# Performance work log

Hardware: AMD Instinct MI355X
Metric: run time of the kernel (lower is better)

The kernel has to match this reference:

```python
import jax, jax.numpy as jnp
import numpy as np

EPS = 1e-6
THRESHOLD = 0.99
MAX_STEPS = 4
MIN_STEPS = 1
N_HEAD = 8
B, N, D, V, L, F, RCF = 1, 256, 512, 32000, 2, 1536, 2048


def rmsnorm(x, w):
    return x * jax.lax.rsqrt(jnp.mean(x * x, axis=-1, keepdims=True) + EPS) * w


def rope(x, base=10000.0):
    # x: [B, N, H, hd] -> rotary embedding (rotate-half convention)
    n, hd = x.shape[1], x.shape[-1]
    half = hd // 2
    inv = 1.0 / (base ** (jnp.arange(half, dtype=jnp.float32) * 2.0 / hd))
    ang = jnp.arange(n, dtype=jnp.float32)[:, None] * inv[None, :]  # [N, half]
    cos = jnp.cos(ang)[None, :, None, :]
    sin = jnp.sin(ang)[None, :, None, :]
    x1, x2 = x[..., :half], x[..., half:]
    return jnp.concatenate([x1 * cos - x2 * sin, x1 * sin + x2 * cos], axis=-1)


def attention(x, wqkv, wo):
    b, n, d = x.shape
    hd = d // N_HEAD
    q, k, v = jnp.split(x @ wqkv, 3, axis=-1)
    q = rope(q.reshape(b, n, N_HEAD, hd))
    k = rope(k.reshape(b, n, N_HEAD, hd))
    v = v.reshape(b, n, N_HEAD, hd)
    scores = jnp.einsum('bqhd,bkhd->bhqk', q, k) / np.float32(np.sqrt(hd))
    causal = jnp.tril(jnp.ones((n, n), dtype=bool))
    scores = jnp.where(causal, scores, jnp.float32(-1e30))
    a = jax.nn.softmax(scores, axis=-1)
    out = jnp.einsum('bhqk,bkhd->bqhd', a, v).reshape(b, n, d)
    return out @ wo


def backbone(input_ids, emb, attn_norm_w, mlp_norm_w, wqkv, wo, w_gate, w_up, w_down, final_norm_w):
    x = emb[input_ids]  # [B, N, D]
    for l in range(L):  # small fixed layer count
        x = x + attention(rmsnorm(x, attn_norm_w[l]), wqkv[l], wo[l])
        h = rmsnorm(x, mlp_norm_w[l])
        x = x + (jax.nn.silu(h @ w_gate[l]) * (h @ w_up[l])) @ w_down[l]  # SwiGLU
    return rmsnorm(x, final_norm_w)


def refinement_step(states, rc_norm_w, rc_w1, rc_w2, w_y, w_delta, w_halt, b_halt):
    h = rmsnorm(states, rc_norm_w)
    y_logits = h @ w_y                                   # [B, N, V]
    refined = states + jax.nn.gelu(h @ rc_w1) @ rc_w2    # [B, N, D]
    delta_logits = rmsnorm(refined, rc_norm_w) @ w_delta # [B, N, V]
    halt = jax.nn.sigmoid(h @ w_halt + b_halt)           # [B, N]
    combined = y_logits + delta_logits                   # compute_prediction
    return combined, halt, refined


def act_combine(halt_probs, step_logits):
    # Vectorized version of the per-(b,n) ACT halting loop.
    # halt_probs: [B, N, S]; step_logits: [B, N, S, V]
    p = halt_probs.at[..., :MIN_STEPS].set(0.0)  # min-step masking (max_steps > min_steps)
    cum = jnp.cumsum(p, axis=-1)
    prev = cum - p                      # exclusive cumulative halting prob
    running = prev < THRESHOLD          # step still executes
    is_last = jnp.arange(p.shape[-1]) == p.shape[-1] - 1
    use_rem = running & ((cum >= THRESHOLD) | is_last)  # halting step gets remainder
    weights = jnp.where(running, jnp.where(use_rem, 1.0 - prev, p), 0.0)
    final = jnp.einsum('bns,bnsv->bnv', weights, step_logits)
    remainder = jnp.sum(jnp.where(use_rem, 1.0 - prev, 0.0), axis=-1)
    ponder = jnp.sum(running, axis=-1).astype(p.dtype) + remainder  # N + R ponder cost
    return final, ponder, weights


def reference(input_ids, emb, attn_norm_w, mlp_norm_w, wqkv, wo, w_gate, w_up, w_down,
              final_norm_w, rc_norm_w, rc_w1, rc_w2, w_y, w_delta, w_halt, b_halt):
    hidden = backbone(input_ids, emb, attn_norm_w, mlp_norm_w, wqkv, wo,
                      w_gate, w_up, w_down, final_norm_w)
    states = hidden
    logits_steps, halt_steps = [], []
    for _ in range(MAX_STEPS):  # fixed refinement unroll
        combined, halt, states = refinement_step(states, rc_norm_w, rc_w1, rc_w2,
                                                 w_y, w_delta, w_halt, b_halt)
        logits_steps.append(combined)
        halt_steps.append(halt)
    step_logits = jnp.stack(logits_steps, axis=2)  # [B, N, S, V]
    halt_probs = jnp.stack(halt_steps, axis=2)     # [B, N, S]
    final_logits, ponder_costs, all_weights = act_combine(halt_probs, step_logits)
    return final_logits, ponder_costs, all_weights


def setup_inputs() -> dict:
    key = jax.random.key(0)
    ks = jax.random.split(key, 16)
    s = 0.02
    return {
        'input_ids': jax.random.randint(ks[0], (B, N), 0, V),
        'emb': jax.random.normal(ks[1], (V, D), jnp.float32) * s,
        'attn_norm_w': jnp.ones((L, D), jnp.float32),
        'mlp_norm_w': jnp.ones((L, D), jnp.float32),
        'wqkv': jax.random.normal(ks[2], (L, D, 3 * D), jnp.float32) * s,
        'wo': jax.random.normal(ks[3], (L, D, D), jnp.float32) * s,
        'w_gate': jax.random.normal(ks[4], (L, D, F), jnp.float32) * s,
        'w_up': jax.random.normal(ks[5], (L, D, F), jnp.float32) * s,
        'w_down': jax.random.normal(ks[6], (L, F, D), jnp.float32) * s,
        'final_norm_w': jnp.ones((D,), jnp.float32),
        'rc_norm_w': jnp.ones((D,), jnp.float32),
        'rc_w1': jax.random.normal(ks[7], (D, RCF), jnp.float32) * s,
        'rc_w2': jax.random.normal(ks[8], (RCF, D), jnp.float32) * s,
        'w_y': jax.random.normal(ks[9], (D, V), jnp.float32) * s,
        'w_delta': jax.random.normal(ks[10], (D, V), jnp.float32) * s,
        'w_halt': jax.random.normal(ks[11], (D,), jnp.float32) * s,
        'b_halt': jnp.zeros((), jnp.float32),
    }
```

## Files before the change

### kernel.cpp

```cpp
#include <hip/hip_runtime.h>
#include <hip/hip_bf16.h>

#define NTOK   256
#define DMODEL 512
#define NHEAD  8
#define HD     64
#define HALF   32
#define FF     1536
#define RCFF   2048
#define VOCAB  32000
#define NLAYER 2
#define NSTEPS 4
#define EPSV   1e-6f
#define THR    0.99f

typedef __attribute__((ext_vector_type(8))) short bf16x8;
typedef __attribute__((ext_vector_type(4))) float f32x4;

__global__ void k_embed(const int* __restrict__ ids, const float* __restrict__ emb,
                        float* __restrict__ x) {
    int row = blockIdx.x;
    int id = ids[row];
    for (int d = threadIdx.x; d < DMODEL; d += blockDim.x)
        x[row * DMODEL + d] = emb[(size_t)id * DMODEL + d];
}

__global__ __launch_bounds__(256) void k_rmsnorm(const float* __restrict__ in,
                                                 const float* __restrict__ w,
                                                 float* __restrict__ out) {
    int row = blockIdx.x;
    const float* xr = in + (size_t)row * DMODEL;
    float s = 0.f;
    for (int d = threadIdx.x; d < DMODEL; d += 256) { float v = xr[d]; s += v * v; }
    __shared__ float red[4];
    int lane = threadIdx.x & 63, wv = threadIdx.x >> 6;
    for (int o = 32; o > 0; o >>= 1) s += __shfl_xor(s, o);
    if (lane == 0) red[wv] = s;
    __syncthreads();
    float tot = red[0] + red[1] + red[2] + red[3];
    float scale = rsqrtf(tot * (1.f / DMODEL) + EPSV);
    for (int d = threadIdx.x; d < DMODEL; d += 256)
        out[(size_t)row * DMODEL + d] = xr[d] * scale * w[d];
}

__global__ __launch_bounds__(256) void k_mm_part(const float* __restrict__ A,
                                                 const float* __restrict__ W,
                                                 float* __restrict__ Cp,
                                                 int K, int N, int kc) {
    __shared__ float As[16][68];
    __shared__ float Ws[16][68];
    const int bn = blockIdx.x * 64;
    const int bm = blockIdx.y * 64;
    const int kz = blockIdx.z * kc;
    const int tx = threadIdx.x & 15;
    const int ty = threadIdx.x >> 4;
    float acc[4][4] = {};
    for (int k0 = kz; k0 < kz + kc; k0 += 16) {
#pragma unroll
        for (int r = 0; r < 4; ++r) {
            int idx = threadIdx.x + r * 256;
            int m = idx >> 4, kk = idx & 15;
            As[kk][m] = A[(size_t)(bm + m) * K + k0 + kk];
            int n = idx & 63, kw = idx >> 6;
            Ws[kw][n] = W[(size_t)(k0 + kw) * N + bn + n];
        }
        __syncthreads();
#pragma unroll
        for (int kk = 0; kk < 16; ++kk) {
            float4 av = *(const float4*)&As[kk][ty * 4];
            float4 bv = *(const float4*)&Ws[kk][tx * 4];
            float a[4] = {av.x, av.y, av.z, av.w};
            float b[4] = {bv.x, bv.y, bv.z, bv.w};
#pragma unroll
            for (int i = 0; i < 4; ++i)
#pragma unroll
                for (int j = 0; j < 4; ++j)
                    acc[i][j] = fmaf(a[i], b[j], acc[i][j]);
        }
        __syncthreads();
    }
    float* cp = Cp + (size_t)blockIdx.z * (size_t)(gridDim.y * 64) * N;
#pragma unroll
    for (int i = 0; i < 4; ++i) {
        int m = bm + ty * 4 + i;
#pragma unroll
        for (int j = 0; j < 4; ++j)
            cp[(size_t)m * N + bn + tx * 4 + j] = acc[i][j];
    }
}

__global__ __launch_bounds__(256) void k_gu_part(const float* __restrict__ A,
                                                 const float* __restrict__ Wg,
                                                 const float* __restrict__ Wu,
                                                 float* __restrict__ GU) {
    __shared__ float As[16][68];
    __shared__ float Ws[16][68];
    const int bn = blockIdx.x * 64;
    const int bm = blockIdx.y * 64;
    const int z = blockIdx.z;
    const float* W = (z >> 2) ? Wu : Wg;
    const int kz = (z & 3) * 128;
    const int tx = threadIdx.x & 15;
    const int ty = threadIdx.x >> 4;
    float acc[4][4] = {};
    for (int k0 = kz; k0 < kz + 128; k0 += 16) {
#pragma unroll
        for (int r = 0; r < 4; ++r) {
            int idx = threadIdx.x + r * 256;
            int m = idx >> 4, kk = idx & 15;
            As[kk][m] = A[(size_t)(bm + m) * DMODEL + k0 + kk];
            int n = idx & 63, kw = idx >> 6;
            Ws[kw][n] = W[(size_t)(k0 + kw) * FF + bn + n];
        }
        __syncthreads();
#pragma unroll
        for (int kk = 0; kk < 16; ++kk) {
            float4 av = *(const float4*)&As[kk][ty * 4];
            float4 bv = *(const float4*)&Ws[kk][tx * 4];
            float a[4] = {av.x, av.y, av.z, av.w};
            float b[4] = {bv.x, bv.y, bv.z, bv.w};
#pragma unroll
            for (int i = 0; i < 4; ++i)
#pragma unroll
                for (int j = 0; j < 4; ++j)
                    acc[i][j] = fmaf(a[i], b[j], acc[i][j]);
        }
        __syncthreads();
    }
    float* cp = GU + (size_t)z * (NTOK * FF);
#pragma unroll
    for (int i = 0; i < 4; ++i) {
        int m = bm + ty * 4 + i;
#pragma unroll
        for (int j = 0; j < 4; ++j)
            cp[(size_t)m * FF + bn + tx * 4 + j] = acc[i][j];
    }
}

__global__ void k_mm_finish(const float* __restrict__ Cp, const float* __restrict__ res,
                            float* __restrict__ C, int tot, int zstride, int nz, int act) {
    int i = blockIdx.x * 256 + threadIdx.x;
    if (i >= tot) return;
    float s = 0.f;
    for (int z = 0; z < nz; ++z) s += Cp[(size_t)z * zstride + i];
    if (res) s += res[i];
    if (act == 1) {
        float xg = s;
        float inner = 0.79788456080286536f * (xg + 0.044715f * xg * xg * xg);
        s = 0.5f * xg * (1.f + tanhf(inner));
    }
    C[i] = s;
}

__global__ void k_finish_silumul(const float* __restrict__ GU, float* __restrict__ C) {
    int i = blockIdx.x * 256 + threadIdx.x;
    float g = 0.f, u = 0.f;
#pragma unroll
    for (int z = 0; z < 4; ++z) {
        g += GU[(size_t)z * (NTOK * FF) + i];
        u += GU[(size_t)(z + 4) * (NTOK * FF) + i];
    }
    float sig = 1.f / (1.f + expf(-g));
    C[i] = g * sig * u;
}

__global__ __launch_bounds__(256) void k_finish_norm(const float* __restrict__ Cp,
                                                     const float* __restrict__ res,
                                                     const float* __restrict__ normw,
                                                     float* __restrict__ out_raw,
                                                     float* __restrict__ out_norm,
                                                     int nz) {
    int row = blockIdx.x, t = threadIdx.x;
    int c0 = t, c1 = t + 256;
    size_t base = (size_t)row * DMODEL;
    float v0 = 0.f, v1 = 0.f;
    for (int z = 0; z < nz; ++z) {
        size_t zb = (size_t)z * (NTOK * DMODEL) + base;
        v0 += Cp[zb + c0];
        v1 += Cp[zb + c1];
    }
    v0 += res[base + c0];
    v1 += res[base + c1];
    float ss = v0 * v0 + v1 * v1;
    __shared__ float red[4];
    int lane = t & 63, wv = t >> 6;
    for (int o = 32; o > 0; o >>= 1) ss += __shfl_xor(ss, o);
    if (lane == 0) red[wv] = ss;
    __syncthreads();
    float tot = red[0] + red[1] + red[2] + red[3];
    float scale = rsqrtf(tot * (1.f / DMODEL) + EPSV);
    out_raw[base + c0] = v0;
    out_raw[base + c1] = v1;
    out_norm[base + c0] = v0 * scale * normw[c0];
    out_norm[base + c1] = v1 * scale * normw[c1];
}

__global__ __launch_bounds__(256) void k_qkv_finish_rope(const float* __restrict__ Cp,
                                                         float* __restrict__ qkv) {
    int pos = blockIdx.x, t = threadIdx.x;
    int h = t >> 5, d = t & 31;
    size_t base = (size_t)pos * FF;
    auto S = [&](int col) {
        float s = 0.f;
#pragma unroll
        for (int z = 0; z < 4; ++z) s += Cp[(size_t)z * (NTOK * FF) + base + col];
        return s;
    };
    int cq0 = h * HD + d, cq1 = cq0 + HALF;
    int ck0 = DMODEL + cq0, ck1 = ck0 + HALF;
    int cv0 = 2 * DMODEL + t, cv1 = cv0 + 256;
    float q0 = S(cq0), q1 = S(cq1);
    float k0 = S(ck0), k1 = S(ck1);
    float v0 = S(cv0), v1 = S(cv1);
    float inv = powf(10000.f, -(float)d / 32.f);
    float ang = (float)pos * inv;
    float c = cosf(ang), s = sinf(ang);
    qkv[base + cq0] = q0 * c - q1 * s;
    qkv[base + cq1] = q0 * s + q1 * c;
    qkv[base + ck0] = k0 * c - k1 * s;
    qkv[base + ck1] = k0 * s + k1 * c;
    qkv[base + cv0] = v0;
    qkv[base + cv1] = v1;
}

__global__ __launch_bounds__(256) void k_attn(const float* __restrict__ qkv,
                                              float* __restrict__ out) {
    int h = blockIdx.x;
    int qi = blockIdx.y;
    int t = threadIdx.x;
    __shared__ float qs[HD];
    __shared__ float ps[NTOK];
    __shared__ float red[4];
    __shared__ float red2[4];
    __shared__ float os[4][HD];
    if (t < HD) qs[t] = qkv[(size_t)qi * FF + h * HD + t];
    __syncthreads();
    float sc = -1e30f;
    if (t <= qi) {
        const float* kr = qkv + (size_t)t * FF + DMODEL + h * HD;
        float s = 0.f;
        for (int d = 0; d < HD; ++d) s = fmaf(qs[d], kr[d], s);
        sc = s * 0.125f;
    }
    float m = sc;
    for (int o = 32; o > 0; o >>= 1) m = fmaxf(m, __shfl_xor(m, o));
    int lane = t & 63, wv = t >> 6;
    if (lane == 0) red[wv] = m;
    __syncthreads();
    m = fmaxf(fmaxf(red[0], red[1]), fmaxf(red[2], red[3]));
    float e = (t <= qi) ? expf(sc - m) : 0.f;
    ps[t] = e;
    float sum = e;
    for (int o = 32; o > 0; o >>= 1) sum += __shfl_xor(sum, o);
    if (lane == 0) red2[wv] = sum;
    __syncthreads();
    sum = red2[0] + red2[1] + red2[2] + red2[3];
    float inv = 1.f / sum;
    int d = t & 63, g = t >> 6;
    float acc = 0.f;
    for (int ki = g; ki <= qi; ki += 4)
        acc = fmaf(ps[ki], qkv[(size_t)ki * FF + 2 * DMODEL + h * HD + d], acc);
    os[g][d] = acc * inv;
    __syncthreads();
    if (t < HD)
        out[(size_t)qi * DMODEL + h * HD + t] = os[0][t] + os[1][t] + os[2][t] + os[3][t];
}

__global__ __launch_bounds__(256) void k_haltactab(const float* __restrict__ H,
                                                   const float* __restrict__ wh,
                                                   const float* __restrict__ bptr,
                                                   float* __restrict__ ponder_out,
                                                   float* __restrict__ w_out,
                                                   __hip_bfloat16* __restrict__ A,
                                                   __hip_bfloat16* __restrict__ Bm) {
    int i = blockIdx.x, t = threadIdx.x;
    int lane = t & 63, wv = t >> 6;
    __shared__ float red[4];
    __shared__ float hvals[3];
    __shared__ float hw[4];
    for (int s = 1; s <= 3; ++s) {
        const float* hr = H + ((size_t)s * NTOK + i) * DMODEL;
        float a = hr[t] * wh[t] + hr[t + 256] * wh[t + 256];
        for (int o = 32; o > 0; o >>= 1) a += __shfl_xor(a, o);
        if (lane == 0) red[wv] = a;
        __syncthreads();
        if (t == 0)
            hvals[s - 1] = 1.f / (1.f + expf(-(red[0] + red[1] + red[2] + red[3] + bptr[0])));
        __syncthreads();
    }
    if (t == 0) {
        float p[4] = {0.f, hvals[0], hvals[1], hvals[2]};
        float cum = 0.f, rem = 0.f;
        int nrun = 0;
#pragma unroll
        for (int s = 0; s < 4; ++s) {
            float prev = cum;
            cum += p[s];
            bool running = prev < THR;
            bool use_rem = running && ((cum >= THR) || (s == 3));
            float v = 0.f;
            if (running) {
                v = use_rem ? (1.f - prev) : p[s];
                if (use_rem) rem += (1.f - prev);
                nrun++;
            }
            hw[s] = v;
            w_out[i * 4 + s] = v;
        }
        ponder_out[i] = (float)nrun + rem;
    }
    __syncthreads();
    float w0 = hw[0], w1 = hw[1], w2 = hw[2], w3 = hw[3];
    size_t base = (size_t)i * DMODEL;
#pragma unroll
    for (int r = 0; r < 2; ++r) {
        int d = t + r * 256;
        float h0 = H[base + d];
        float h1 = H[(size_t)(NTOK * DMODEL) + base + d];
        float h2 = H[(size_t)(2 * NTOK * DMODEL) + base + d];
        float h3 = H[(size_t)(3 * NTOK * DMODEL) + base + d];
        float h4 = H[(size_t)(4 * NTOK * DMODEL) + base + d];
        A[base + d]  = __float2bfloat16(w0 * h0 + w1 * h1 + w2 * h2 + w3 * h3);
        Bm[base + d] = __float2bfloat16(w0 * h1 + w1 * h2 + w2 * h3 + w3 * h4);
    }
}

__global__ __launch_bounds__(512) void k_logits_mfma(const __hip_bfloat16* __restrict__ Abf,
                                                     const __hip_bfloat16* __restrict__ Bbf,
                                                     const float* __restrict__ Wy,
                                                     const float* __restrict__ Wd,
                                                     float* __restrict__ out) {
    __shared__ short Alds[256 * 32];
    __shared__ short Blds[256 * 32];
    __shared__ short Wys[32 * 70];
    __shared__ short Wds[32 * 70];
    const int tid  = threadIdx.x;
    const int wave = tid >> 6;
    const int lane = tid & 63;
    const int wrow = (wave & 1) * 128;
    const int wcol = (wave >> 1) * 16;
    const int cl   = lane & 15;
    const int kg   = lane >> 4;
    const int col  = blockIdx.x * 64 + wcol + cl;

    const int kr = tid >> 4;
    const int c4 = (tid & 15) * 4;
    const int sr0 = tid >> 2;
    const int skp = (tid & 3) * 8;

    f32x4 acc[8];
#pragma unroll
    for (int i = 0; i < 8; ++i) acc[i] = (f32x4){0.f, 0.f, 0.f, 0.f};

    const float* gy = Wy + (size_t)kr * VOCAB + blockIdx.x * 64 + c4;
    const float* gd = Wd + (size_t)kr * VOCAB + blockIdx.x * 64 + c4;

    float4 ry = *(const float4*)gy;
    float4 rd = *(const float4*)gd;
    bf16x8 ra0 = *(const bf16x8*)(Abf + (size_t)sr0 * DMODEL + skp);
    bf16x8 ra1 = *(const bf16x8*)(Abf + (size_t)(sr0 + 128) * DMODEL + skp);
    bf16x8 rb0 = *(const bf16x8*)(Bbf + (size_t)sr0 * DMODEL + skp);
    bf16x8 rb1 = *(const bf16x8*)(Bbf + (size_t)(sr0 + 128) * DMODEL + skp);

    for (int t = 0; t < 16; ++t) {
        __syncthreads();
        {
            short2 a, b;
            a.x = (short)__hip_bfloat16_raw(__float2bfloat16(ry.x)).x;
            a.y = (short)__hip_bfloat16_raw(__float2bfloat16(ry.y)).x;
            b.x = (short)__hip_bfloat16_raw(__float2bfloat16(ry.z)).x;
            b.y = (short)__hip_bfloat16_raw(__float2bfloat16(ry.w)).x;
            *(short2*)&Wys[kr * 70 + c4]     = a;
            *(short2*)&Wys[kr * 70 + c4 + 2] = b;
            a.x = (short)__hip_bfloat16_raw(__float2bfloat16(rd.x)).x;
            a.y = (short)__hip_bfloat16_raw(__float2bfloat16(rd.y)).x;
            b.x = (short)__hip_bfloat16_raw(__float2bfloat16(rd.z)).x;
            b.y = (short)__hip_bfloat16_raw(__float2bfloat16(rd.w)).x;
            *(short2*)&Wds[kr * 70 + c4]     = a;
            *(short2*)&Wds[kr * 70 + c4 + 2] = b;
            *(bf16x8*)&Alds[sr0 * 32 + skp]         = ra0;
            *(bf16x8*)&Alds[(sr0 + 128) * 32 + skp] = ra1;
            *(bf16x8*)&Blds[sr0 * 32 + skp]         = rb0;
            *(bf16x8*)&Blds[(sr0 + 128) * 32 + skp] = rb1;
        }
        if (t < 15) {
            const int kn = (t + 1) * 32;
            ry  = *(const float4*)(gy + (size_t)(t + 1) * 32 * VOCAB);
            rd  = *(const float4*)(gd + (size_t)(t + 1) * 32 * VOCAB);
            ra0 = *(const bf16x8*)(Abf + (size_t)sr0 * DMODEL + kn + skp);
            ra1 = *(const bf16x8*)(Abf + (size_t)(sr0 + 128) * DMODEL + kn + skp);
            rb0 = *(const bf16x8*)(Bbf + (size_t)sr0 * DMODEL + kn + skp);
            rb1 = *(const bf16x8*)(Bbf + (size_t)(sr0 + 128) * DMODEL + kn + skp);
        }
        __syncthreads();
        bf16x8 wy, wd;
#pragma unroll
        for (int j = 0; j < 8; ++j) {
            wy[j] = Wys[(kg * 8 + j) * 70 + wcol + cl];
            wd[j] = Wds[(kg * 8 + j) * 70 + wcol + cl];
        }
#pragma unroll
        for (int mt = 0; mt < 8; ++mt) {
            const int row = wrow + mt * 16 + cl;
            const bf16x8 a = *(const bf16x8*)&Alds[row * 32 + kg * 8];
            const bf16x8 b = *(const bf16x8*)&Blds[row * 32 + kg * 8];
            acc[mt] = __builtin_amdgcn_mfma_f32_16x16x32_bf16(a, wy, acc[mt], 0, 0, 0);
            acc[mt] = __builtin_amdgcn_mfma_f32_16x16x32_bf16(b, wd, acc[mt], 0, 0, 0);
        }
    }
#pragma unroll
    for (int mt = 0; mt < 8; ++mt)
#pragma unroll
        for (int r = 0; r < 4; ++r)
            out[(size_t)(wrow + mt * 16 + kg * 4 + r) * VOCAB + col] = acc[mt][r];
}

extern "C" void kernel_launch(void* const* d_in, const int* in_sizes, int n_in,
                              void* d_out, int out_size, void* d_ws, size_t ws_size,
                              hipStream_t stream) {
    const int*   ids          = (const int*)d_in[0];
    const float* emb          = (const float*)d_in[1];
    const float* attn_norm_w  = (const float*)d_in[2];
    const float* mlp_norm_w   = (const float*)d_in[3];
    const float* wqkv         = (const float*)d_in[4];
    const float* wo           = (const float*)d_in[5];
    const float* w_gate       = (const float*)d_in[6];
    const float* w_up         = (const float*)d_in[7];
    const float* w_down       = (const float*)d_in[8];
    const float* final_norm_w = (const float*)d_in[9];
    const float* rc_norm_w    = (const float*)d_in[10];
    const float* rc_w1        = (const float*)d_in[11];
    const float* rc_w2        = (const float*)d_in[12];
    const float* w_y          = (const float*)d_in[13];
    const float* w_delta      = (const float*)d_in[14];
    const float* w_halt       = (const float*)d_in[15];
    const float* b_halt       = (const float*)d_in[16];
    float* out = (float*)d_out;

    float* ws = (float*)d_ws;
    float* x       = ws + 0;
    float* xn      = ws + 131072;
    float* qkv     = ws + 262144;
    float* attnout = ws + 655360;
    float* g       = ws + 786432;
    float* t1      = ws + 1179648;
    float* states  = ws + 1703936;
    float* states2 = ws + 1835008;
    float* H       = ws + 1966080;
    __hip_bfloat16* Abf = (__hip_bfloat16*)(ws + 2623488);
    __hip_bfloat16* Bbf = (__hip_bfloat16*)(ws + 2754560);
    float* Cp      = ws + 2885632;
    float* GU      = ws + 1179648;

    k_embed<<<NTOK, 256, 0, stream>>>(ids, emb, x);
    k_rmsnorm<<<NTOK, 256, 0, stream>>>(x, attn_norm_w, xn);
    for (int l = 0; l < NLAYER; ++l) {
        k_mm_part<<<dim3(FF / 64, 4, 4), 256, 0, stream>>>(
            xn, wqkv + (size_t)l * DMODEL * FF, Cp, DMODEL, FF, 128);
        k_qkv_finish_rope<<<NTOK, 256, 0, stream>>>(Cp, qkv);
        k_attn<<<dim3(NHEAD, NTOK), 256, 0, stream>>>(qkv, attnout);
        k_mm_part<<<dim3(DMODEL / 64, 4, 8), 256, 0, stream>>>(
            attnout, wo + (size_t)l * DMODEL * DMODEL, Cp, DMODEL, DMODEL, 64);
        k_finish_norm<<<NTOK, 256, 0, stream>>>(Cp, x, mlp_norm_w + l * DMODEL, x, xn, 8);
        k_gu_part<<<dim3(FF / 64, 4, 8), 256, 0, stream>>>(
            xn, w_gate + (size_t)l * DMODEL * FF, w_up + (size_t)l * DMODEL * FF, GU);
        k_finish_silumul<<<NTOK * FF / 256, 256, 0, stream>>>(GU, g);
        k_mm_part<<<dim3(DMODEL / 64, 4, 12), 256, 0, stream>>>(
            g, w_down + (size_t)l * FF * DMODEL, Cp, FF, DMODEL, 128);
        const float* nw = (l == 0) ? (attn_norm_w + DMODEL) : final_norm_w;
        float* nout = (l == 0) ? xn : states;
        k_finish_norm<<<NTOK, 256, 0, stream>>>(Cp, x, nw, x, nout, 12);
    }

    k_rmsnorm<<<NTOK, 256, 0, stream>>>(states, rc_norm_w, H);
    float* scur = states;
    float* snxt = states2;
    for (int s = 0; s < NSTEPS; ++s) {
        k_mm_part<<<dim3(RCFF / 64, 4, 4), 256, 0, stream>>>(
            H + (size_t)s * NTOK * DMODEL, rc_w1, Cp, DMODEL, RCFF, 128);
        k_mm_finish<<<NTOK * RCFF / 256, 256, 0, stream>>>(
            Cp, nullptr, t1, NTOK * RCFF, NTOK * RCFF, 4, 1);
        k_mm_part<<<dim3(DMODEL / 64, 4, 16), 256, 0, stream>>>(
            t1, rc_w2, Cp, RCFF, DMODEL, 128);
        k_finish_norm<<<NTOK, 256, 0, stream>>>(
            Cp, scur, rc_norm_w, snxt, H + (size_t)(s + 1) * NTOK * DMODEL, 16);
        float* tmp = scur; scur = snxt; snxt = tmp;
    }

    k_haltactab<<<NTOK, 256, 0, stream>>>(H, w_halt, b_halt,
                                          out + (size_t)NTOK * VOCAB,
                                          out + (size_t)NTOK * VOCAB + NTOK,
                                          Abf, Bbf);

    k_logits_mfma<<<VOCAB / 64, 512, 0, stream>>>(Abf, Bbf, w_y, w_delta, out);
}
```

Before: 382.3 us.

## Prefetch next k-tile into registers in fp32 GEMMs, fuse embed+norm, halve GU split-K

The fp32 split-K GEMM kernels now load the next 16-wide k-slice into registers while the current slice is computed from LDS, so global latency overlaps with FMA work. The embedding gather is fused with the first RMSNorm, which saves one launch and one pass over x. The gate/up GEMM split-K factor drops from 4 to 2, halving the partial buffers the SiLU-multiply finish must read. The cost is more registers per thread and fewer blocks in the gate/up grid.

```diff
diff --git a/kernel.cpp b/kernel.cpp
--- a/kernel.cpp
+++ b/kernel.cpp
@@ -17,12 +17,28 @@
 typedef __attribute__((ext_vector_type(8))) short bf16x8;
 typedef __attribute__((ext_vector_type(4))) float f32x4;
 
-__global__ void k_embed(const int* __restrict__ ids, const float* __restrict__ emb,
-                        float* __restrict__ x) {
-    int row = blockIdx.x;
+__global__ __launch_bounds__(256) void k_embed_norm(const int* __restrict__ ids,
+                                                    const float* __restrict__ emb,
+                                                    const float* __restrict__ w,
+                                                    float* __restrict__ x,
+                                                    float* __restrict__ xn) {
+    int row = blockIdx.x, t = threadIdx.x;
     int id = ids[row];
-    for (int d = threadIdx.x; d < DMODEL; d += blockDim.x)
-        x[row * DMODEL + d] = emb[(size_t)id * DMODEL + d];
+    const float* er = emb + (size_t)id * DMODEL;
+    float v0 = er[t], v1 = er[t + 256];
+    float ss = v0 * v0 + v1 * v1;
+    __shared__ float red[4];
+    int lane = t & 63, wv = t >> 6;
+    for (int o = 32; o > 0; o >>= 1) ss += __shfl_xor(ss, o);
+    if (lane == 0) red[wv] = ss;
+    __syncthreads();
+    float tot = red[0] + red[1] + red[2] + red[3];
+    float scale = rsqrtf(tot * (1.f / DMODEL) + EPSV);
+    size_t base = (size_t)row * DMODEL;
+    x[base + t] = v0;
+    x[base + t + 256] = v1;
+    xn[base + t] = v0 * scale * w[t];
+    xn[base + t + 256] = v1 * scale * w[t + 256];
 }
 
 __global__ __launch_bounds__(256) void k_rmsnorm(const float* __restrict__ in,
@@ -54,17 +70,36 @@
     const int kz = blockIdx.z * kc;
     const int tx = threadIdx.x & 15;
     const int ty = threadIdx.x >> 4;
+    float ar[4], wr[4];
+#pragma unroll
+    for (int r = 0; r < 4; ++r) {
+        int idx = threadIdx.x + r * 256;
+        int m = idx >> 4, kk = idx & 15;
+        ar[r] = A[(size_t)(bm + m) * K + kz + kk];
+        int n = idx & 63, kw = idx >> 6;
+        wr[r] = W[(size_t)(kz + kw) * N + bn + n];
+    }
     float acc[4][4] = {};
     for (int k0 = kz; k0 < kz + kc; k0 += 16) {
 #pragma unroll
         for (int r = 0; r < 4; ++r) {
             int idx = threadIdx.x + r * 256;
             int m = idx >> 4, kk = idx & 15;
-            As[kk][m] = A[(size_t)(bm + m) * K + k0 + kk];
+            As[kk][m] = ar[r];
             int n = idx & 63, kw = idx >> 6;
-            Ws[kw][n] = W[(size_t)(k0 + kw) * N + bn + n];
-        }
-        __syncthreads();
+            Ws[kw][n] = wr[r];
+        }
+        __syncthreads();
+        if (k0 + 16 < kz + kc) {
+#pragma unroll
+            for (int r = 0; r < 4; ++r) {
+                int idx = threadIdx.x + r * 256;
+                int m = idx >> 4, kk = idx & 15;
+                ar[r] = A[(size_t)(bm + m) * K + k0 + 16 + kk];
+                int n = idx & 63, kw = idx >> 6;
+                wr[r] = W[(size_t)(k0 + 16 + kw) * N + bn + n];
+            }
+        }
 #pragma unroll
         for (int kk = 0; kk < 16; ++kk) {
             float4 av = *(const float4*)&As[kk][ty * 4];
@@ -98,21 +133,40 @@
     const int bn = blockIdx.x * 64;
     const int bm = blockIdx.y * 64;
     const int z = blockIdx.z;
-    const float* W = (z >> 2) ? Wu : Wg;
-    const int kz = (z & 3) * 128;
+    const float* W = (z >> 1) ? Wu : Wg;
+    const int kz = (z & 1) * 256;
     const int tx = threadIdx.x & 15;
     const int ty = threadIdx.x >> 4;
+    float ar[4], wr[4];
+#pragma unroll
+    for (int r = 0; r < 4; ++r) {
+        int idx = threadIdx.x + r * 256;
+        int m = idx >> 4, kk = idx & 15;
+        ar[r] = A[(size_t)(bm + m) * DMODEL + kz + kk];
+        int n = idx & 63, kw = idx >> 6;
+        wr[r] = W[(size_t)(kz + kw) * FF + bn + n];
+    }
     float acc[4][4] = {};
-    for (int k0 = kz; k0 < kz + 128; k0 += 16) {
+    for (int k0 = kz; k0 < kz + 256; k0 += 16) {
 #pragma unroll
         for (int r = 0; r < 4; ++r) {
             int idx = threadIdx.x + r * 256;
             int m = idx >> 4, kk = idx & 15;
-            As[kk][m] = A[(size_t)(bm + m) * DMODEL + k0 + kk];
+            As[kk][m] = ar[r];
             int n = idx & 63, kw = idx >> 6;
-            Ws[kw][n] = W[(size_t)(k0 + kw) * FF + bn + n];
-        }
-        __syncthreads();
+            Ws[kw][n] = wr[r];
+        }
+        __syncthreads();
+        if (k0 + 16 < kz + 256) {
+#pragma unroll
+            for (int r = 0; r < 4; ++r) {
+                int idx = threadIdx.x + r * 256;
+                int m = idx >> 4, kk = idx & 15;
+                ar[r] = A[(size_t)(bm + m) * DMODEL + k0 + 16 + kk];
+                int n = idx & 63, kw = idx >> 6;
+                wr[r] = W[(size_t)(k0 + 16 + kw) * FF + bn + n];
+            }
+        }
 #pragma unroll
         for (int kk = 0; kk < 16; ++kk) {
             float4 av = *(const float4*)&As[kk][ty * 4];
@@ -154,12 +208,8 @@
 
 __global__ void k_finish_silumul(const float* __restrict__ GU, float* __restrict__ C) {
     int i = blockIdx.x * 256 + threadIdx.x;
-    float g = 0.f, u = 0.f;
-#pragma unroll
-    for (int z = 0; z < 4; ++z) {
-        g += GU[(size_t)z * (NTOK * FF) + i];
-        u += GU[(size_t)(z + 4) * (NTOK * FF) + i];
-    }
+    float g = GU[i] + GU[(size_t)(NTOK * FF) + i];
+    float u = GU[(size_t)(2 * NTOK * FF) + i] + GU[(size_t)(3 * NTOK * FF) + i];
     float sig = 1.f / (1.f + expf(-g));
     C[i] = g * sig * u;
 }
@@ -403,9 +453,9 @@
         for (int mt = 0; mt < 8; ++mt) {
             const int row = wrow + mt * 16 + cl;
             const bf16x8 a = *(const bf16x8*)&Alds[row * 32 + kg * 8];
-            const bf16x8 b = *(const bf16x8*)&Blds[row * 32 + kg * 8];
+            const bf16x8 bb = *(const bf16x8*)&Blds[row * 32 + kg * 8];
             acc[mt] = __builtin_amdgcn_mfma_f32_16x16x32_bf16(a, wy, acc[mt], 0, 0, 0);
-            acc[mt] = __builtin_amdgcn_mfma_f32_16x16x32_bf16(b, wd, acc[mt], 0, 0, 0);
+            acc[mt] = __builtin_amdgcn_mfma_f32_16x16x32_bf16(bb, wd, acc[mt], 0, 0, 0);
         }
     }
 #pragma unroll
@@ -452,8 +502,7 @@
     float* Cp      = ws + 2885632;
     float* GU      = ws + 1179648;
 
-    k_embed<<<NTOK, 256, 0, stream>>>(ids, emb, x);
-    k_rmsnorm<<<NTOK, 256, 0, stream>>>(x, attn_norm_w, xn);
+    k_embed_norm<<<NTOK, 256, 0, stream>>>(ids, emb, attn_norm_w, x, xn);
     for (int l = 0; l < NLAYER; ++l) {
         k_mm_part<<<dim3(FF / 64, 4, 4), 256, 0, stream>>>(
             xn, wqkv + (size_t)l * DMODEL * FF, Cp, DMODEL, FF, 128);
@@ -462,7 +511,7 @@
         k_mm_part<<<dim3(DMODEL / 64, 4, 8), 256, 0, stream>>>(
             attnout, wo + (size_t)l * DMODEL * DMODEL, Cp, DMODEL, DMODEL, 64);
         k_finish_norm<<<NTOK, 256, 0, stream>>>(Cp, x, mlp_norm_w + l * DMODEL, x, xn, 8);
-        k_gu_part<<<dim3(FF / 64, 4, 8), 256, 0, stream>>>(
+        k_gu_part<<<dim3(FF / 64, 4, 4), 256, 0, stream>>>(
             xn, w_gate + (size_t)l * DMODEL * FF, w_up + (size_t)l * DMODEL * FF, GU);
         k_finish_silumul<<<NTOK * FF / 256, 256, 0, stream>>>(GU, g);
         k_mm_part<<<dim3(DMODEL / 64, 4, 12), 256, 0, stream>>>(
```

After: 374.8 us. 1.02x faster.
